# Performance work log

Measured on AMD Instinct MI355X. Metric: run time of the kernel, lower is better.

The kernel has to match this reference:

```python
import jax, jax.numpy as jnp
import numpy as np

N_NODES = 50000
N_EDGES = 800000
IN_DIM = 128
HID = 256
HEADS = 4
OUT_DIM = 128
NEG_SLOPE = 0.2


def gat_conv(x, src, dst, W, a_src, a_dst, b, heads, out_ch):
    """PyG-style GATConv: per-edge attention + segment softmax over dst."""
    N = x.shape[0]
    h = (x @ W).reshape(N, heads, out_ch)              # [N,H,C]
    alph_s = jnp.einsum('nhc,hc->nh', h, a_src)        # [N,H]
    alph_d = jnp.einsum('nhc,hc->nh', h, a_dst)        # [N,H]
    e = jax.nn.leaky_relu(alph_s[src] + alph_d[dst], NEG_SLOPE)  # [E,H]
    m = jax.lax.stop_gradient(jax.ops.segment_max(e, dst, num_segments=N))
    ex = jnp.exp(e - m[dst])
    s = jax.ops.segment_sum(ex, dst, num_segments=N)
    alpha = ex / (s[dst] + 1e-16)                      # [E,H]
    out = jax.ops.segment_sum(h[src] * alpha[:, :, None], dst, num_segments=N)
    return out.reshape(N, heads * out_ch) + b


def setup_inputs() -> dict:
    key = jax.random.key(0)
    ks = jax.random.split(key, 12)
    x = jax.random.normal(ks[0], (N_NODES, IN_DIM), dtype=jnp.float32)
    edge_index = jax.random.randint(ks[1], (2, N_EDGES), 0, N_NODES, dtype=jnp.int64)
    c1 = HID // HEADS  # 64
    sc1 = 1.0 / np.sqrt(IN_DIM)
    sc2 = 1.0 / np.sqrt(HID)
    W1 = jax.random.normal(ks[2], (IN_DIM, HID), dtype=jnp.float32) * sc1
    a1_src = jax.random.normal(ks[3], (HEADS, c1), dtype=jnp.float32) * sc1
    a1_dst = jax.random.normal(ks[4], (HEADS, c1), dtype=jnp.float32) * sc1
    b1 = jnp.zeros((HID,), dtype=jnp.float32)
    W2 = jax.random.normal(ks[5], (HID, OUT_DIM), dtype=jnp.float32) * sc2
    a2_src = jax.random.normal(ks[6], (1, OUT_DIM), dtype=jnp.float32) * sc2
    a2_dst = jax.random.normal(ks[7], (1, OUT_DIM), dtype=jnp.float32) * sc2
    b2 = jnp.zeros((OUT_DIM,), dtype=jnp.float32)
    return {"x": x, "edge_index": edge_index, "W1": W1, "a1_src": a1_src,
            "a1_dst": a1_dst, "b1": b1, "W2": W2, "a2_src": a2_src,
            "a2_dst": a2_dst, "b2": b2}


def reference(x, edge_index, W1, a1_src, a1_dst, b1, W2, a2_src, a2_dst, b2):
    N = x.shape[0]
    loops = jnp.arange(N, dtype=edge_index.dtype)
    # PyG default add_self_loops=True
    src = jnp.concatenate([edge_index[0], loops])
    dst = jnp.concatenate([edge_index[1], loops])
    h = jax.nn.relu(gat_conv(x, src, dst, W1, a1_src, a1_dst, b1, HEADS, HID // HEADS))
    # dropout is identity in eval mode
    return gat_conv(h, src, dst, W2, a2_src, a2_dst, b2, 1, OUT_DIM)
```

## Files before the change

kernel.cpp:

```cpp
#include <hip/hip_runtime.h>
#include <math.h>

#define NEG_SLOPE 0.2f
#define SLOTS 64
#define ECAP 63
#define NBMAX 391
#define BCAP 2432

typedef __attribute__((ext_vector_type(8))) short bf16x8;
typedef __attribute__((ext_vector_type(4))) float f32x4;
typedef __attribute__((ext_vector_type(2))) float f32x2;

__device__ __forceinline__ float lrelu(float t) {
    return t > 0.f ? t : NEG_SLOPE * t;
}
__device__ __forceinline__ unsigned short f2bf(float f) {
    unsigned u = __float_as_uint(f);
    unsigned r = (u + 0x7fff + ((u >> 16) & 1)) >> 16;
    return (unsigned short)r;
}
__device__ __forceinline__ f32x2 unpack2(unsigned v) {
    f32x2 r;
    r.x = __uint_as_float(v << 16);
    r.y = __uint_as_float(v & 0xffff0000u);
    return r;
}

__global__ void prep0(const float* __restrict__ W1, const float* __restrict__ a1s,
                      const float* __restrict__ a1d, float* __restrict__ vsd1,
                      const float* __restrict__ W2, const float* __restrict__ a2s,
                      const float* __restrict__ a2d, float* __restrict__ vsd2) {
    int i = blockIdx.x * 256 + threadIdx.x;
    if (i < 512) {
        int k = i >> 2, h = i & 3;
        float s = 0.f, d = 0.f;
        for (int c = 0; c < 64; c++) {
            float wv = W1[k * 256 + h * 64 + c];
            s += wv * a1s[h * 64 + c];
            d += wv * a1d[h * 64 + c];
        }
        vsd1[h * 128 + k] = s;
        vsd1[(4 + h) * 128 + k] = d;
    } else if (i < 768) {
        int j = i - 512;
        float s = 0.f, d = 0.f;
        for (int c = 0; c < 128; c++) {
            float wv = W2[j * 128 + c];
            s += wv * a2s[c];
            d += wv * a2d[c];
        }
        vsd2[j] = s;
        vsd2[256 + j] = d;
    }
}

#define EMIT(dd, ss)                                                     \
    {                                                                    \
        int bk_ = (dd) >> 7;                                             \
        int pos_ = atomicAdd(&cntS[bk_], 1);                             \
        if (pos_ < BCAP)                                                 \
            bin[(size_t)bk_ * BCAP + pos_] =                             \
                ((unsigned)((dd) & 127) << 16) | (unsigned)(ss);         \
    }

__global__ void mega(const int* __restrict__ src, const int* __restrict__ dst,
                     int* __restrict__ gcur, unsigned* __restrict__ bin,
                     const float* __restrict__ x, uint4* __restrict__ xb4,
                     const float* __restrict__ W1, unsigned short* __restrict__ W1t,
                     const float* __restrict__ W2, unsigned short* __restrict__ W2t,
                     const float* __restrict__ vsd1,
                     float* __restrict__ as1, float* __restrict__ ad1,
                     int E, int N, int nb, int bP1, int bC, int bW1, int bW2) {
    __shared__ float vs[1024];
    __shared__ int cntS[NBMAX];
    const int b = blockIdx.x, t = threadIdx.x;
    if (b < bP1) {
        for (int i = t; i < nb; i += 256) cntS[i] = 0;
        __syncthreads();
        const int4* s4p = (const int4*)src;
        const int4* d4p = (const int4*)dst;
        const int E4 = E >> 2;
        int4 sv[4], dv[4];
        bool act[4];
#pragma unroll
        for (int i = 0; i < 4; i++) {
            int idx = b * 1024 + i * 256 + t;
            act[i] = idx < E4;
            sv[i] = act[i] ? s4p[idx] : (int4){0, 0, 0, 0};
            dv[i] = act[i] ? d4p[idx] : (int4){0, 0, 0, 0};
        }
        int exd = -1, exs = 0;
        if (b == 0 && (E4 << 2) + t < E) {
            exd = dst[(E4 << 2) + t];
            exs = src[(E4 << 2) + t];
        }
#pragma unroll
        for (int i = 0; i < 4; i++)
            if (act[i]) {
                atomicAdd(&cntS[dv[i].x >> 7], 1);
                atomicAdd(&cntS[dv[i].y >> 7], 1);
                atomicAdd(&cntS[dv[i].z >> 7], 1);
                atomicAdd(&cntS[dv[i].w >> 7], 1);
            }
        if (exd >= 0) atomicAdd(&cntS[exd >> 7], 1);
        __syncthreads();
        for (int i = t; i < nb; i += 256) {
            int c = cntS[i];
            cntS[i] = c ? atomicAdd(&gcur[i], c) : 0;
        }
        __syncthreads();
#pragma unroll
        for (int i = 0; i < 4; i++)
            if (act[i]) {
                EMIT(dv[i].x, sv[i].x);
                EMIT(dv[i].y, sv[i].y);
                EMIT(dv[i].z, sv[i].z);
                EMIT(dv[i].w, sv[i].w);
            }
        if (exd >= 0) EMIT(exd, exs);
    } else if (b < bC) {
        int i = (b - bP1) * 256 + t;
        if (i < N * 16) {
            const float4* x4 = (const float4*)x;
            float4 v0 = x4[2 * i], v1 = x4[2 * i + 1];
            uint4 o;
            o.x = (unsigned)f2bf(v0.x) | ((unsigned)f2bf(v0.y) << 16);
            o.y = (unsigned)f2bf(v0.z) | ((unsigned)f2bf(v0.w) << 16);
            o.z = (unsigned)f2bf(v1.x) | ((unsigned)f2bf(v1.y) << 16);
            o.w = (unsigned)f2bf(v1.z) | ((unsigned)f2bf(v1.w) << 16);
            xb4[i] = o;
        }
    } else if (b < bW1) {
        int i = (b - bC) * 256 + t;
        int n = i >> 7, k = i & 127;
        W1t[i] = f2bf(W1[k * 256 + n]);
    } else if (b < bW2) {
        int i = (b - bW1) * 256 + t;
        int n = i >> 8, k = i & 255;
        W2t[i] = f2bf(W2[k * 128 + n]);
    } else {
        for (int i = t; i < 1024; i += 256) vs[i] = vsd1[i];
        __syncthreads();
        int wave = t >> 6, lane = t & 63;
        int n = (b - bW2) * 4 + wave;
        if (n >= N) return;
        float acc[8];
#pragma unroll
        for (int j = 0; j < 8; j++) acc[j] = 0.f;
#pragma unroll
        for (int i = 0; i < 2; i++) {
            float xv = x[(size_t)n * 128 + i * 64 + lane];
#pragma unroll
            for (int j = 0; j < 8; j++) acc[j] += xv * vs[j * 128 + i * 64 + lane];
        }
#pragma unroll
        for (int off = 32; off > 0; off >>= 1) {
#pragma unroll
            for (int j = 0; j < 8; j++) acc[j] += __shfl_down(acc[j], off, 64);
        }
        if (lane == 0) {
#pragma unroll
            for (int h = 0; h < 4; h++) {
                as1[n * 4 + h] = acc[h];
                ad1[n * 4 + h] = acc[4 + h];
            }
        }
    }
}

__global__ __launch_bounds__(256) void build_csr(const int* __restrict__ gcur,
                                                 const unsigned* __restrict__ bin,
                                                 unsigned short* __restrict__ eSrc,
                                                 int* __restrict__ cursor) {
    __shared__ unsigned short slotS[128 * 64];
    __shared__ int lc[128];
    const int b = blockIdx.x, t = threadIdx.x;
    if (t < 128) lc[t] = 0;
    __syncthreads();
    int cnt = gcur[b];
    if (cnt > BCAP) cnt = BCAP;
    const unsigned* bb = bin + (size_t)b * BCAP;
    for (int i = t; i < cnt; i += 256) {
        unsigned e = bb[i];
        int dl = e >> 16;
        int p = atomicAdd(&lc[dl], 1);
        if (p < ECAP) slotS[(dl << 6) + p] = (unsigned short)(e & 0xffff);
    }
    __syncthreads();
    const uint4* sp = (const uint4*)slotS;
    uint4* dp = (uint4*)(eSrc + ((size_t)b << 13));
#pragma unroll
    for (int i = 0; i < 4; i++) dp[t + i * 256] = sp[t + i * 256];
    if (t < 128) cursor[(b << 7) + t] = lc[t];
}

template <int K, int N>
__global__ __launch_bounds__(256) void gemm_mfma(const unsigned short* __restrict__ A,
                                                 const unsigned short* __restrict__ Bt,
                                                 unsigned short* __restrict__ Cb, int M) {
    constexpr int LDT = 72;
    __shared__ __align__(16) short As[128 * LDT];
    __shared__ __align__(16) short Bs[64 * LDT];
    const int t = threadIdx.x;
    const int wave = t >> 6, lane = t & 63;
    const int row0 = blockIdx.x * 128;
    const int n0 = blockIdx.y * 64;

    f32x4 acc[2][4];
#pragma unroll
    for (int mt = 0; mt < 2; mt++)
#pragma unroll
        for (int nt = 0; nt < 4; nt++) acc[mt][nt] = (f32x4){0.f, 0.f, 0.f, 0.f};

    const int r = t >> 3, c8 = (t & 7) * 8;
    for (int kc = 0; kc < K; kc += 64) {
        const unsigned short* srcA = A + (size_t)row0 * K + kc;
#pragma unroll
        for (int p = 0; p < 4; p++) {
            int rr = r + p * 32;
            *(bf16x8*)&As[rr * LDT + c8] = *(const bf16x8*)&srcA[(size_t)rr * K + c8];
        }
        const unsigned short* srcB = Bt + (size_t)n0 * K + kc;
#pragma unroll
        for (int p = 0; p < 2; p++) {
            int rr = r + p * 32;
            *(bf16x8*)&Bs[rr * LDT + c8] = *(const bf16x8*)&srcB[(size_t)rr * K + c8];
        }
        __syncthreads();

        const int mbase = wave * 32 + (lane & 15);
        const int quad = lane >> 4;
#pragma unroll
        for (int ks = 0; ks < 2; ks++) {
            int ko = ks * 32 + quad * 8;
            bf16x8 a0 = *(const bf16x8*)&As[mbase * LDT + ko];
            bf16x8 a1 = *(const bf16x8*)&As[(mbase + 16) * LDT + ko];
#pragma unroll
            for (int nt = 0; nt < 4; nt++) {
                bf16x8 b = *(const bf16x8*)&Bs[((lane & 15) + nt * 16) * LDT + ko];
                acc[0][nt] = __builtin_amdgcn_mfma_f32_16x16x32_bf16(a0, b, acc[0][nt], 0, 0, 0);
                acc[1][nt] = __builtin_amdgcn_mfma_f32_16x16x32_bf16(a1, b, acc[1][nt], 0, 0, 0);
            }
        }
        __syncthreads();
    }

    const int colb = n0 + (lane & 15);
    const int rquad = (lane >> 4) * 4;
#pragma unroll
    for (int mt = 0; mt < 2; mt++) {
        int rb = row0 + wave * 32 + mt * 16 + rquad;
#pragma unroll
        for (int nt = 0; nt < 4; nt++) {
#pragma unroll
            for (int rr2 = 0; rr2 < 4; rr2++) {
                int row = rb + rr2;
                if (row < M) Cb[(size_t)row * N + colb + nt * 16] = f2bf(acc[mt][nt][rr2]);
            }
        }
    }
}

__global__ __launch_bounds__(256) void gemm1_head(
    const unsigned short* __restrict__ agg, const unsigned short* __restrict__ W1t,
    const float* __restrict__ b1, const float* __restrict__ vsd2,
    unsigned short* __restrict__ out1b, float* __restrict__ as2, float* __restrict__ ad2,
    int M, int Mpad) {
    constexpr int K = 128, LDT = 72;
    __shared__ __align__(16) short As[128 * LDT];
    __shared__ __align__(16) short Bs[64 * LDT];
    const int t = threadIdx.x;
    const int wave = t >> 6, lane = t & 63;
    const int row0 = blockIdx.x * 128;
    const int h = blockIdx.y;
    const unsigned short* A = agg + (size_t)h * Mpad * K;
    const unsigned short* Bt = W1t + (size_t)h * 64 * K;

    f32x4 acc[2][4];
#pragma unroll
    for (int mt = 0; mt < 2; mt++)
#pragma unroll
        for (int nt = 0; nt < 4; nt++) acc[mt][nt] = (f32x4){0.f, 0.f, 0.f, 0.f};

    const int r = t >> 3, c8 = (t & 7) * 8;
    for (int kc = 0; kc < K; kc += 64) {
        const unsigned short* srcA = A + (size_t)row0 * K + kc;
#pragma unroll
        for (int p = 0; p < 4; p++) {
            int rr = r + p * 32;
            *(bf16x8*)&As[rr * LDT + c8] = *(const bf16x8*)&srcA[(size_t)rr * K + c8];
        }
        const unsigned short* srcB = Bt + kc;
#pragma unroll
        for (int p = 0; p < 2; p++) {
            int rr = r + p * 32;
            *(bf16x8*)&Bs[rr * LDT + c8] = *(const bf16x8*)&srcB[(size_t)rr * K + c8];
        }
        __syncthreads();

        const int mbase = wave * 32 + (lane & 15);
        const int quad = lane >> 4;
#pragma unroll
        for (int ks = 0; ks < 2; ks++) {
            int ko = ks * 32 + quad * 8;
            bf16x8 a0 = *(const bf16x8*)&As[mbase * LDT + ko];
            bf16x8 a1 = *(const bf16x8*)&As[(mbase + 16) * LDT + ko];
#pragma unroll
            for (int nt = 0; nt < 4; nt++) {
                bf16x8 b = *(const bf16x8*)&Bs[((lane & 15) + nt * 16) * LDT + ko];
                acc[0][nt] = __builtin_amdgcn_mfma_f32_16x16x32_bf16(a0, b, acc[0][nt], 0, 0, 0);
                acc[1][nt] = __builtin_amdgcn_mfma_f32_16x16x32_bf16(a1, b, acc[1][nt], 0, 0, 0);
            }
        }
        __syncthreads();
    }

    const int col16 = lane & 15;
    const int grp = lane >> 4;
#pragma unroll
    for (int mt = 0; mt < 2; mt++) {
        int rb = row0 + wave * 32 + mt * 16 + grp * 4;
#pragma unroll
        for (int rr = 0; rr < 4; rr++) {
            int row = rb + rr;
            float ps = 0.f, pd = 0.f;
#pragma unroll
            for (int nt = 0; nt < 4; nt++) {
                int cg = h * 64 + col16 + nt * 16;
                float rres = acc[mt][nt][rr] + b1[cg];
                rres = fmaxf(rres, 0.f);
                if (row < M) out1b[(size_t)row * 256 + cg] = f2bf(rres);
                ps += rres * vsd2[cg];
                pd += rres * vsd2[256 + cg];
            }
#pragma unroll
            for (int mask = 1; mask < 16; mask <<= 1) {
                ps += __shfl_xor(ps, mask, 64);
                pd += __shfl_xor(pd, mask, 64);
            }
            if (col16 == 0 && row < M) {
                atomicAdd(&as2[row], ps);
                atomicAdd(&ad2[row], pd);
            }
        }
    }
}

__global__ __launch_bounds__(256) void fused_gather1(
    const int* __restrict__ cursor, const unsigned short* __restrict__ eSrc,
    const unsigned short* __restrict__ Xb,
    const float* __restrict__ as_, const float* __restrict__ ad_,
    unsigned short* __restrict__ agg, int N, int Mpad) {
    const int wv = threadIdx.x >> 6, lane = threadIdx.x & 63;
    const int half = lane >> 5, hl = lane & 31;
    const int d = blockIdx.x * 8 + wv * 2 + half;

    __shared__ float4 alS[4][2][64];
    __shared__ int offS[4][2][64];

    const bool vn = d < N;
    int deg = 0;
    if (vn) { deg = cursor[d]; if (deg > ECAP) deg = ECAP; }
    float4 adv = make_float4(0.f, 0.f, 0.f, 0.f);
    if (vn) adv = ((const float4*)ad_)[d];

    const int beg = d << 6;
    const int j0 = hl, j1 = hl + 32;
    const bool a0 = vn && (j0 <= deg), a1 = vn && (j1 <= deg);
    int s0 = vn ? d : 0, s1 = vn ? d : 0;
    if (vn && j0 < deg) s0 = eSrc[beg + j0];
    if (vn && j1 < deg) s1 = eSrc[beg + j1];
    float4 q0 = make_float4(0.f, 0.f, 0.f, 0.f), q1 = q0;
    if (a0) q0 = ((const float4*)as_)[s0];
    if (a1) q1 = ((const float4*)as_)[s1];

    float qa0[4] = {q0.x, q0.y, q0.z, q0.w};
    float qa1[4] = {q1.x, q1.y, q1.z, q1.w};
    float ad4[4] = {adv.x, adv.y, adv.z, adv.w};
    float e0[4], e1[4], m[4];
#pragma unroll
    for (int h = 0; h < 4; h++) {
        e0[h] = a0 ? lrelu(qa0[h] + ad4[h]) : -1e30f;
        e1[h] = a1 ? lrelu(qa1[h] + ad4[h]) : -1e30f;
        m[h] = fmaxf(e0[h], e1[h]);
    }
#pragma unroll
    for (int off = 1; off < 32; off <<= 1)
#pragma unroll
        for (int h = 0; h < 4; h++) m[h] = fmaxf(m[h], __shfl_xor(m[h], off, 64));
    float x0[4], x1[4], sum[4];
#pragma unroll
    for (int h = 0; h < 4; h++) {
        x0[h] = a0 ? __expf(e0[h] - m[h]) : 0.f;
        x1[h] = a1 ? __expf(e1[h] - m[h]) : 0.f;
        sum[h] = x0[h] + x1[h];
    }
#pragma unroll
    for (int off = 1; off < 32; off <<= 1)
#pragma unroll
        for (int h = 0; h < 4; h++) sum[h] += __shfl_xor(sum[h], off, 64);
    float ri[4];
#pragma unroll
    for (int h = 0; h < 4; h++) ri[h] = 1.f / (sum[h] + 1e-16f);

    alS[wv][half][j0] = make_float4(x0[0] * ri[0], x0[1] * ri[1], x0[2] * ri[2], x0[3] * ri[3]);
    alS[wv][half][j1] = make_float4(x1[0] * ri[0], x1[1] * ri[1], x1[2] * ri[2], x1[3] * ri[3]);
    offS[wv][half][j0] = s0 << 8;
    offS[wv][half][j1] = s1 << 8;

    int rows = vn ? deg + 1 : 0;
    { int o = __shfl_xor(rows, 32, 64); rows = rows > o ? rows : o; }

    const char* Xc = (const char*)Xb;
    const int myoff = hl * 8;
    f32x2 acc[4][2];
#pragma unroll
    for (int h = 0; h < 4; h++) { acc[h][0] = (f32x2){0.f, 0.f}; acc[h][1] = (f32x2){0.f, 0.f}; }

    int j = 0;
    for (; j + 3 < rows; j += 4) {
        int o0 = offS[wv][half][j], o1 = offS[wv][half][j + 1];
        int o2 = offS[wv][half][j + 2], o3 = offS[wv][half][j + 3];
        uint2 v0 = *(const uint2*)(Xc + o0 + myoff);
        uint2 v1 = *(const uint2*)(Xc + o1 + myoff);
        uint2 v2 = *(const uint2*)(Xc + o2 + myoff);
        uint2 v3 = *(const uint2*)(Xc + o3 + myoff);
        float4 al0 = alS[wv][half][j];
        float4 al1 = alS[wv][half][j + 1];
        float4 al2 = alS[wv][half][j + 2];
        float4 al3 = alS[wv][half][j + 3];
        {
            f32x2 lo = unpack2(v0.x), hi = unpack2(v0.y);
            acc[0][0] += al0.x * lo; acc[0][1] += al0.x * hi;
            acc[1][0] += al0.y * lo; acc[1][1] += al0.y * hi;
            acc[2][0] += al0.z * lo; acc[2][1] += al0.z * hi;
            acc[3][0] += al0.w * lo; acc[3][1] += al0.w * hi;
        }
        {
            f32x2 lo = unpack2(v1.x), hi = unpack2(v1.y);
            acc[0][0] += al1.x * lo; acc[0][1] += al1.x * hi;
            acc[1][0] += al1.y * lo; acc[1][1] += al1.y * hi;
            acc[2][0] += al1.z * lo; acc[2][1] += al1.z * hi;
            acc[3][0] += al1.w * lo; acc[3][1] += al1.w * hi;
        }
        {
            f32x2 lo = unpack2(v2.x), hi = unpack2(v2.y);
            acc[0][0] += al2.x * lo; acc[0][1] += al2.x * hi;
            acc[1][0] += al2.y * lo; acc[1][1] += al2.y * hi;
            acc[2][0] += al2.z * lo; acc[2][1] += al2.z * hi;
            acc[3][0] += al2.w * lo; acc[3][1] += al2.w * hi;
        }
        {
            f32x2 lo = unpack2(v3.x), hi = unpack2(v3.y);
            acc[0][0] += al3.x * lo; acc[0][1] += al3.x * hi;
            acc[1][0] += al3.y * lo; acc[1][1] += al3.y * hi;
            acc[2][0] += al3.z * lo; acc[2][1] += al3.z * hi;
            acc[3][0] += al3.w * lo; acc[3][1] += al3.w * hi;
        }
    }
    for (; j < rows; j++) {
        int o0 = offS[wv][half][j];
        uint2 v0 = *(const uint2*)(Xc + o0 + myoff);
        float4 al0 = alS[wv][half][j];
        f32x2 lo = unpack2(v0.x), hi = unpack2(v0.y);
        acc[0][0] += al0.x * lo; acc[0][1] += al0.x * hi;
        acc[1][0] += al0.y * lo; acc[1][1] += al0.y * hi;
        acc[2][0] += al0.z * lo; acc[2][1] += al0.z * hi;
        acc[3][0] += al0.w * lo; acc[3][1] += al0.w * hi;
    }

    if (vn) {
#pragma unroll
        for (int h = 0; h < 4; h++) {
            uint2 pack;
            pack.x = (unsigned)f2bf(acc[h][0].x) | ((unsigned)f2bf(acc[h][0].y) << 16);
            pack.y = (unsigned)f2bf(acc[h][1].x) | ((unsigned)f2bf(acc[h][1].y) << 16);
            ((uint2*)(agg + ((size_t)h * Mpad + d) * 128))[hl] = pack;
        }
    }
}

__global__ __launch_bounds__(256) void fused_gather2(
    const int* __restrict__ cursor, const unsigned short* __restrict__ eSrc,
    const unsigned short* __restrict__ Hb,
    const float* __restrict__ as_, const float* __restrict__ ad_,
    const float* __restrict__ b2, float* __restrict__ out, int N) {
    const int wv = threadIdx.x >> 6, lane = threadIdx.x & 63;
    const int half = lane >> 5, hl = lane & 31;
    const int d = blockIdx.x * 8 + wv * 2 + half;

    __shared__ float alS[4][2][64];
    __shared__ int offS[4][2][64];

    const bool vn = d < N;
    int deg = 0;
    if (vn) { deg = cursor[d]; if (deg > ECAP) deg = ECAP; }
    const float adv = vn ? ad_[d] : 0.f;

    const int beg = d << 6;
    const int j0 = hl, j1 = hl + 32;
    const bool a0 = vn && (j0 <= deg), a1 = vn && (j1 <= deg);
    int s0 = vn ? d : 0, s1 = vn ? d : 0;
    if (vn && j0 < deg) s0 = eSrc[beg + j0];
    if (vn && j1 < deg) s1 = eSrc[beg + j1];
    float e0 = a0 ? lrelu(as_[s0] + adv) : -1e30f;
    float e1 = a1 ? lrelu(as_[s1] + adv) : -1e30f;
    float m = fmaxf(e0, e1);
#pragma unroll
    for (int off = 1; off < 32; off <<= 1) m = fmaxf(m, __shfl_xor(m, off, 64));
    float x0 = a0 ? __expf(e0 - m) : 0.f;
    float x1 = a1 ? __expf(e1 - m) : 0.f;
    float sum = x0 + x1;
#pragma unroll
    for (int off = 1; off < 32; off <<= 1) sum += __shfl_xor(sum, off, 64);
    float ri = 1.f / (sum + 1e-16f);

    alS[wv][half][j0] = x0 * ri;
    alS[wv][half][j1] = x1 * ri;
    offS[wv][half][j0] = s0 << 8;
    offS[wv][half][j1] = s1 << 8;

    int rows = vn ? deg + 1 : 0;
    { int o = __shfl_xor(rows, 32, 64); rows = rows > o ? rows : o; }

    const char* Hc = (const char*)Hb;
    const int myoff = hl * 8;
    f32x2 acc0 = (f32x2){0.f, 0.f}, acc1 = (f32x2){0.f, 0.f};

    int j = 0;
    for (; j + 3 < rows; j += 4) {
        int o0 = offS[wv][half][j], o1 = offS[wv][half][j + 1];
        int o2 = offS[wv][half][j + 2], o3 = offS[wv][half][j + 3];
        uint2 v0 = *(const uint2*)(Hc + o0 + myoff);
        uint2 v1 = *(const uint2*)(Hc + o1 + myoff);
        uint2 v2 = *(const uint2*)(Hc + o2 + myoff);
        uint2 v3 = *(const uint2*)(Hc + o3 + myoff);
        float b0 = alS[wv][half][j], b1v = alS[wv][half][j + 1];
        float b2v = alS[wv][half][j + 2], b3 = alS[wv][half][j + 3];
        acc0 += b0 * unpack2(v0.x); acc1 += b0 * unpack2(v0.y);
        acc0 += b1v * unpack2(v1.x); acc1 += b1v * unpack2(v1.y);
        acc0 += b2v * unpack2(v2.x); acc1 += b2v * unpack2(v2.y);
        acc0 += b3 * unpack2(v3.x); acc1 += b3 * unpack2(v3.y);
    }
    for (; j < rows; j++) {
        int o0 = offS[wv][half][j];
        uint2 v0 = *(const uint2*)(Hc + o0 + myoff);
        float b0 = alS[wv][half][j];
        acc0 += b0 * unpack2(v0.x); acc1 += b0 * unpack2(v0.y);
    }

    if (vn) {
        float4 bb = ((const float4*)b2)[hl];
        float4 o;
        o.x = acc0.x + bb.x;
        o.y = acc0.y + bb.y;
        o.z = acc1.x + bb.z;
        o.w = acc1.y + bb.w;
        ((float4*)(out + (size_t)d * 128))[hl] = o;
    }
}

extern "C" void kernel_launch(void* const* d_in, const int* in_sizes, int n_in,
                              void* d_out, int out_size, void* d_ws, size_t ws_size,
                              hipStream_t stream) {
    const float* x   = (const float*)d_in[0];
    const int*   ei  = (const int*)d_in[1];
    const float* W1  = (const float*)d_in[2];
    const float* a1s = (const float*)d_in[3];
    const float* a1d = (const float*)d_in[4];
    const float* b1  = (const float*)d_in[5];
    const float* W2  = (const float*)d_in[6];
    const float* a2s = (const float*)d_in[7];
    const float* a2d = (const float*)d_in[8];
    const float* b2  = (const float*)d_in[9];

    const int N = in_sizes[0] / 128;
    const int E = in_sizes[1] / 2;
    const int* srcIdx = ei;
    const int* dstIdx = ei + E;
    float* out = (float*)d_out;

    const int MT = (N + 127) / 128;
    const int M_pad = MT * 128;
    const int nb = (N + 127) >> 7;

    char* w = (char*)d_ws;
    unsigned short* x_bf  = (unsigned short*)w; w += (size_t)N * 128 * 2;
    unsigned short* agg   = (unsigned short*)w; w += (size_t)4 * M_pad * 128 * 2;
    unsigned short* out1b = (unsigned short*)w; w += (size_t)M_pad * 256 * 2;
    unsigned short* h2b   = (unsigned short*)w; w += (size_t)N * 128 * 2;
    unsigned short* W1t   = (unsigned short*)w; w += (size_t)128 * 256 * 2;
    unsigned short* W2t   = (unsigned short*)w; w += (size_t)256 * 128 * 2;
    float* vsd1 = (float*)w; w += (size_t)128 * 8 * 4;
    float* vsd2 = (float*)w; w += (size_t)256 * 2 * 4;
    float* as1  = (float*)w; w += (size_t)N * 4 * 4;
    float* ad1  = (float*)w; w += (size_t)N * 4 * 4;
    float* as2  = (float*)w; w += (size_t)N * 4;
    float* ad2  = (float*)w; w += (size_t)N * 4;
    int* cursor = (int*)w;  w += (size_t)M_pad * 4;
    unsigned short* eSrc = (unsigned short*)w; w += (size_t)M_pad * SLOTS * 2;
    int* gcur = (int*)w; w += (size_t)nb * 4;
    unsigned* bin = (unsigned*)agg;

    hipMemsetAsync(gcur, 0, (size_t)nb * 4, stream);
    hipMemsetAsync(as2, 0, (size_t)N * 4, stream);
    hipMemsetAsync(ad2, 0, (size_t)N * 4, stream);

    prep0<<<3, 256, 0, stream>>>(W1, a1s, a1d, vsd1, W2, a2s, a2d, vsd2);

    {
        const int bP1 = (E / 4 + 1023) / 1024;
        const int nC  = (N * 16 + 255) / 256;
        const int bC  = bP1 + nC;
        const int bW1 = bC + 128;
        const int bW2 = bW1 + 128;
        const int nG  = (N + 3) / 4;
        mega<<<bW2 + nG, 256, 0, stream>>>(srcIdx, dstIdx, gcur, bin,
                                           x, (uint4*)x_bf, W1, W1t, W2, W2t,
                                           vsd1, as1, ad1, E, N, nb, bP1, bC, bW1, bW2);
    }

    build_csr<<<nb, 256, 0, stream>>>(gcur, bin, eSrc, cursor);

    fused_gather1<<<(N + 7) / 8, 256, 0, stream>>>(cursor, eSrc, x_bf, as1, ad1, agg, N, M_pad);
    gemm1_head<<<dim3(MT, 4), 256, 0, stream>>>(agg, W1t, b1, vsd2, out1b, as2, ad2, N, M_pad);

    gemm_mfma<256, 128><<<dim3(MT, 2), 256, 0, stream>>>(out1b, W2t, h2b, N);
    fused_gather2<<<(N + 7) / 8, 256, 0, stream>>>(cursor, eSrc, h2b, as2, ad2, b2, out, N);
}
```

Before: 249.1 us.

## Fuse layer-1 gather with its head GEMM and shrink edge-binning blocks

Merges the layer-1 attention gather and the per-head W1 GEMM into one kernel. Each block gathers 32 destination rows for all four heads into shared memory, then runs MFMA against W1t read directly from global memory, with the bias, ReLU and layer-2 attention projections in the epilogue. This removes the round trip through the 4×Mpad×128 bf16 agg buffer and one kernel launch, so the edge bin now aliases out1b. The edge-binning part of the mega kernel also moves from four int4 per thread to one, which quadruples the block count and the number of global atomics on gcur in exchange for more parallelism.

```diff
diff --git a/kernel.cpp b/kernel.cpp
--- a/kernel.cpp
+++ b/kernel.cpp
@@ -80,28 +80,21 @@
         const int4* s4p = (const int4*)src;
         const int4* d4p = (const int4*)dst;
         const int E4 = E >> 2;
-        int4 sv[4], dv[4];
-        bool act[4];
-#pragma unroll
-        for (int i = 0; i < 4; i++) {
-            int idx = b * 1024 + i * 256 + t;
-            act[i] = idx < E4;
-            sv[i] = act[i] ? s4p[idx] : (int4){0, 0, 0, 0};
-            dv[i] = act[i] ? d4p[idx] : (int4){0, 0, 0, 0};
-        }
+        const int idx = b * 256 + t;
+        const bool act = idx < E4;
+        int4 sv = act ? s4p[idx] : (int4){0, 0, 0, 0};
+        int4 dv = act ? d4p[idx] : (int4){0, 0, 0, 0};
         int exd = -1, exs = 0;
         if (b == 0 && (E4 << 2) + t < E) {
             exd = dst[(E4 << 2) + t];
             exs = src[(E4 << 2) + t];
         }
-#pragma unroll
-        for (int i = 0; i < 4; i++)
-            if (act[i]) {
-                atomicAdd(&cntS[dv[i].x >> 7], 1);
-                atomicAdd(&cntS[dv[i].y >> 7], 1);
-                atomicAdd(&cntS[dv[i].z >> 7], 1);
-                atomicAdd(&cntS[dv[i].w >> 7], 1);
-            }
+        if (act) {
+            atomicAdd(&cntS[dv.x >> 7], 1);
+            atomicAdd(&cntS[dv.y >> 7], 1);
+            atomicAdd(&cntS[dv.z >> 7], 1);
+            atomicAdd(&cntS[dv.w >> 7], 1);
+        }
         if (exd >= 0) atomicAdd(&cntS[exd >> 7], 1);
         __syncthreads();
         for (int i = t; i < nb; i += 256) {
@@ -109,14 +102,12 @@
             cntS[i] = c ? atomicAdd(&gcur[i], c) : 0;
         }
         __syncthreads();
-#pragma unroll
-        for (int i = 0; i < 4; i++)
-            if (act[i]) {
-                EMIT(dv[i].x, sv[i].x);
-                EMIT(dv[i].y, sv[i].y);
-                EMIT(dv[i].z, sv[i].z);
-                EMIT(dv[i].w, sv[i].w);
-            }
+        if (act) {
+            EMIT(dv.x, sv.x);
+            EMIT(dv.y, sv.y);
+            EMIT(dv.z, sv.z);
+            EMIT(dv.w, sv.w);
+        }
         if (exd >= 0) EMIT(exd, exs);
     } else if (b < bC) {
         int i = (b - bP1) * 256 + t;
@@ -194,6 +185,202 @@
     if (t < 128) cursor[(b << 7) + t] = lc[t];
 }
 
+__global__ __launch_bounds__(256) void gather_gemm1(
+    const int* __restrict__ cursor, const unsigned short* __restrict__ eSrc,
+    const unsigned short* __restrict__ Xb,
+    const float* __restrict__ as_, const float* __restrict__ ad_,
+    const unsigned short* __restrict__ W1t, const float* __restrict__ b1,
+    const float* __restrict__ vsd2,
+    unsigned short* __restrict__ out1b, float* __restrict__ as2,
+    float* __restrict__ ad2, int N) {
+    constexpr int LDT = 136;
+    __shared__ __align__(16) short As[128 * LDT];
+    __shared__ float4 alS[4][2][64];
+    __shared__ int offS[4][2][64];
+    const int t = threadIdx.x;
+    const int wv = t >> 6, lane = t & 63;
+    const int half = lane >> 5, hl = lane & 31;
+    const int row0 = blockIdx.x * 32;
+
+    for (int pass = 0; pass < 4; pass++) {
+        const int ln = pass * 8 + wv * 2 + half;
+        const int d = row0 + ln;
+        const bool vn = d < N;
+        int deg = 0;
+        if (vn) { deg = cursor[d]; if (deg > ECAP) deg = ECAP; }
+        float4 adv = make_float4(0.f, 0.f, 0.f, 0.f);
+        if (vn) adv = ((const float4*)ad_)[d];
+
+        const int beg = d << 6;
+        const int j0 = hl, j1 = hl + 32;
+        const bool a0 = vn && (j0 <= deg), a1 = vn && (j1 <= deg);
+        int s0 = vn ? d : 0, s1 = vn ? d : 0;
+        if (vn && j0 < deg) s0 = eSrc[beg + j0];
+        if (vn && j1 < deg) s1 = eSrc[beg + j1];
+        float4 q0 = make_float4(0.f, 0.f, 0.f, 0.f), q1 = q0;
+        if (a0) q0 = ((const float4*)as_)[s0];
+        if (a1) q1 = ((const float4*)as_)[s1];
+
+        float qa0[4] = {q0.x, q0.y, q0.z, q0.w};
+        float qa1[4] = {q1.x, q1.y, q1.z, q1.w};
+        float ad4[4] = {adv.x, adv.y, adv.z, adv.w};
+        float e0[4], e1[4], m[4];
+#pragma unroll
+        for (int h = 0; h < 4; h++) {
+            e0[h] = a0 ? lrelu(qa0[h] + ad4[h]) : -1e30f;
+            e1[h] = a1 ? lrelu(qa1[h] + ad4[h]) : -1e30f;
+            m[h] = fmaxf(e0[h], e1[h]);
+        }
+#pragma unroll
+        for (int off = 1; off < 32; off <<= 1)
+#pragma unroll
+            for (int h = 0; h < 4; h++) m[h] = fmaxf(m[h], __shfl_xor(m[h], off, 64));
+        float x0[4], x1[4], sum[4];
+#pragma unroll
+        for (int h = 0; h < 4; h++) {
+            x0[h] = a0 ? __expf(e0[h] - m[h]) : 0.f;
+            x1[h] = a1 ? __expf(e1[h] - m[h]) : 0.f;
+            sum[h] = x0[h] + x1[h];
+        }
+#pragma unroll
+        for (int off = 1; off < 32; off <<= 1)
+#pragma unroll
+            for (int h = 0; h < 4; h++) sum[h] += __shfl_xor(sum[h], off, 64);
+        float ri[4];
+#pragma unroll
+        for (int h = 0; h < 4; h++) ri[h] = 1.f / (sum[h] + 1e-16f);
+
+        alS[wv][half][j0] = make_float4(x0[0] * ri[0], x0[1] * ri[1], x0[2] * ri[2], x0[3] * ri[3]);
+        alS[wv][half][j1] = make_float4(x1[0] * ri[0], x1[1] * ri[1], x1[2] * ri[2], x1[3] * ri[3]);
+        offS[wv][half][j0] = s0 << 8;
+        offS[wv][half][j1] = s1 << 8;
+
+        int rows = vn ? deg + 1 : 0;
+        { int o = __shfl_xor(rows, 32, 64); rows = rows > o ? rows : o; }
+
+        const char* Xc = (const char*)Xb;
+        const int myoff = hl * 8;
+        f32x2 acc[4][2];
+#pragma unroll
+        for (int h = 0; h < 4; h++) { acc[h][0] = (f32x2){0.f, 0.f}; acc[h][1] = (f32x2){0.f, 0.f}; }
+
+        int j = 0;
+        for (; j + 3 < rows; j += 4) {
+            int o0 = offS[wv][half][j], o1 = offS[wv][half][j + 1];
+            int o2 = offS[wv][half][j + 2], o3 = offS[wv][half][j + 3];
+            uint2 v0 = *(const uint2*)(Xc + o0 + myoff);
+            uint2 v1 = *(const uint2*)(Xc + o1 + myoff);
+            uint2 v2 = *(const uint2*)(Xc + o2 + myoff);
+            uint2 v3 = *(const uint2*)(Xc + o3 + myoff);
+            float4 al0 = alS[wv][half][j];
+            float4 al1 = alS[wv][half][j + 1];
+            float4 al2 = alS[wv][half][j + 2];
+            float4 al3 = alS[wv][half][j + 3];
+            {
+                f32x2 lo = unpack2(v0.x), hi = unpack2(v0.y);
+                acc[0][0] += al0.x * lo; acc[0][1] += al0.x * hi;
+                acc[1][0] += al0.y * lo; acc[1][1] += al0.y * hi;
+                acc[2][0] += al0.z * lo; acc[2][1] += al0.z * hi;
+                acc[3][0] += al0.w * lo; acc[3][1] += al0.w * hi;
+            }
+            {
+                f32x2 lo = unpack2(v1.x), hi = unpack2(v1.y);
+                acc[0][0] += al1.x * lo; acc[0][1] += al1.x * hi;
+                acc[1][0] += al1.y * lo; acc[1][1] += al1.y * hi;
+                acc[2][0] += al1.z * lo; acc[2][1] += al1.z * hi;
+                acc[3][0] += al1.w * lo; acc[3][1] += al1.w * hi;
+            }
+            {
+                f32x2 lo = unpack2(v2.x), hi = unpack2(v2.y);
+                acc[0][0] += al2.x * lo; acc[0][1] += al2.x * hi;
+                acc[1][0] += al2.y * lo; acc[1][1] += al2.y * hi;
+                acc[2][0] += al2.z * lo; acc[2][1] += al2.z * hi;
+                acc[3][0] += al2.w * lo; acc[3][1] += al2.w * hi;
+            }
+            {
+                f32x2 lo = unpack2(v3.x), hi = unpack2(v3.y);
+                acc[0][0] += al3.x * lo; acc[0][1] += al3.x * hi;
+                acc[1][0] += al3.y * lo; acc[1][1] += al3.y * hi;
+                acc[2][0] += al3.z * lo; acc[2][1] += al3.z * hi;
+                acc[3][0] += al3.w * lo; acc[3][1] += al3.w * hi;
+            }
+        }
+        for (; j < rows; j++) {
+            int o0 = offS[wv][half][j];
+            uint2 v0 = *(const uint2*)(Xc + o0 + myoff);
+            float4 al0 = alS[wv][half][j];
+            f32x2 lo = unpack2(v0.x), hi = unpack2(v0.y);
+            acc[0][0] += al0.x * lo; acc[0][1] += al0.x * hi;
+            acc[1][0] += al0.y * lo; acc[1][1] += al0.y * hi;
+            acc[2][0] += al0.z * lo; acc[2][1] += al0.z * hi;
+            acc[3][0] += al0.w * lo; acc[3][1] += al0.w * hi;
+        }
+
+        if (vn) {
+#pragma unroll
+            for (int h = 0; h < 4; h++) {
+                uint2 pack;
+                pack.x = (unsigned)f2bf(acc[h][0].x) | ((unsigned)f2bf(acc[h][0].y) << 16);
+                pack.y = (unsigned)f2bf(acc[h][1].x) | ((unsigned)f2bf(acc[h][1].y) << 16);
+                ((uint2*)&As[(h * 32 + ln) * LDT])[hl] = pack;
+            }
+        }
+    }
+    __syncthreads();
+
+    const int h = wv;
+    const short* Ah = &As[h * 32 * LDT];
+    const unsigned short* Bh = W1t + (size_t)h * 64 * 128;
+    const int l16 = lane & 15, quad = lane >> 4;
+
+    f32x4 acc[2][4];
+#pragma unroll
+    for (int mt = 0; mt < 2; mt++)
+#pragma unroll
+        for (int nt = 0; nt < 4; nt++) acc[mt][nt] = (f32x4){0.f, 0.f, 0.f, 0.f};
+
+#pragma unroll
+    for (int ks = 0; ks < 4; ks++) {
+        const int ko = ks * 32 + quad * 8;
+        bf16x8 a0 = *(const bf16x8*)&Ah[l16 * LDT + ko];
+        bf16x8 a1 = *(const bf16x8*)&Ah[(16 + l16) * LDT + ko];
+#pragma unroll
+        for (int nt = 0; nt < 4; nt++) {
+            bf16x8 b = *(const bf16x8*)&Bh[(size_t)(nt * 16 + l16) * 128 + ko];
+            acc[0][nt] = __builtin_amdgcn_mfma_f32_16x16x32_bf16(a0, b, acc[0][nt], 0, 0, 0);
+            acc[1][nt] = __builtin_amdgcn_mfma_f32_16x16x32_bf16(a1, b, acc[1][nt], 0, 0, 0);
+        }
+    }
+
+#pragma unroll
+    for (int mt = 0; mt < 2; mt++) {
+        int rb = row0 + mt * 16 + quad * 4;
+#pragma unroll
+        for (int rr = 0; rr < 4; rr++) {
+            int row = rb + rr;
+            float ps = 0.f, pd = 0.f;
+#pragma unroll
+            for (int nt = 0; nt < 4; nt++) {
+                int cg = h * 64 + l16 + nt * 16;
+                float rres = acc[mt][nt][rr] + b1[cg];
+                rres = fmaxf(rres, 0.f);
+                if (row < N) out1b[(size_t)row * 256 + cg] = f2bf(rres);
+                ps += rres * vsd2[cg];
+                pd += rres * vsd2[256 + cg];
+            }
+#pragma unroll
+            for (int mask = 1; mask < 16; mask <<= 1) {
+                ps += __shfl_xor(ps, mask, 64);
+                pd += __shfl_xor(pd, mask, 64);
+            }
+            if (l16 == 0 && row < N) {
+                atomicAdd(&as2[row], ps);
+                atomicAdd(&ad2[row], pd);
+            }
+        }
+    }
+}
+
 template <int K, int N>
 __global__ __launch_bounds__(256) void gemm_mfma(const unsigned short* __restrict__ A,
                                                  const unsigned short* __restrict__ Bt,
@@ -257,225 +444,6 @@
                 int row = rb + rr2;
                 if (row < M) Cb[(size_t)row * N + colb + nt * 16] = f2bf(acc[mt][nt][rr2]);
             }
-        }
-    }
-}
-
-__global__ __launch_bounds__(256) void gemm1_head(
-    const unsigned short* __restrict__ agg, const unsigned short* __restrict__ W1t,
-    const float* __restrict__ b1, const float* __restrict__ vsd2,
-    unsigned short* __restrict__ out1b, float* __restrict__ as2, float* __restrict__ ad2,
-    int M, int Mpad) {
-    constexpr int K = 128, LDT = 72;
-    __shared__ __align__(16) short As[128 * LDT];
-    __shared__ __align__(16) short Bs[64 * LDT];
-    const int t = threadIdx.x;
-    const int wave = t >> 6, lane = t & 63;
-    const int row0 = blockIdx.x * 128;
-    const int h = blockIdx.y;
-    const unsigned short* A = agg + (size_t)h * Mpad * K;
-    const unsigned short* Bt = W1t + (size_t)h * 64 * K;
-
-    f32x4 acc[2][4];
-#pragma unroll
-    for (int mt = 0; mt < 2; mt++)
-#pragma unroll
-        for (int nt = 0; nt < 4; nt++) acc[mt][nt] = (f32x4){0.f, 0.f, 0.f, 0.f};
-
-    const int r = t >> 3, c8 = (t & 7) * 8;
-    for (int kc = 0; kc < K; kc += 64) {
-        const unsigned short* srcA = A + (size_t)row0 * K + kc;
-#pragma unroll
-        for (int p = 0; p < 4; p++) {
-            int rr = r + p * 32;
-            *(bf16x8*)&As[rr * LDT + c8] = *(const bf16x8*)&srcA[(size_t)rr * K + c8];
-        }
-        const unsigned short* srcB = Bt + kc;
-#pragma unroll
-        for (int p = 0; p < 2; p++) {
-            int rr = r + p * 32;
-            *(bf16x8*)&Bs[rr * LDT + c8] = *(const bf16x8*)&srcB[(size_t)rr * K + c8];
-        }
-        __syncthreads();
-
-        const int mbase = wave * 32 + (lane & 15);
-        const int quad = lane >> 4;
-#pragma unroll
-        for (int ks = 0; ks < 2; ks++) {
-            int ko = ks * 32 + quad * 8;
-            bf16x8 a0 = *(const bf16x8*)&As[mbase * LDT + ko];
-            bf16x8 a1 = *(const bf16x8*)&As[(mbase + 16) * LDT + ko];
-#pragma unroll
-            for (int nt = 0; nt < 4; nt++) {
-                bf16x8 b = *(const bf16x8*)&Bs[((lane & 15) + nt * 16) * LDT + ko];
-                acc[0][nt] = __builtin_amdgcn_mfma_f32_16x16x32_bf16(a0, b, acc[0][nt], 0, 0, 0);
-                acc[1][nt] = __builtin_amdgcn_mfma_f32_16x16x32_bf16(a1, b, acc[1][nt], 0, 0, 0);
-            }
-        }
-        __syncthreads();
-    }
-
-    const int col16 = lane & 15;
-    const int grp = lane >> 4;
-#pragma unroll
-    for (int mt = 0; mt < 2; mt++) {
-        int rb = row0 + wave * 32 + mt * 16 + grp * 4;
-#pragma unroll
-        for (int rr = 0; rr < 4; rr++) {
-            int row = rb + rr;
-            float ps = 0.f, pd = 0.f;
-#pragma unroll
-            for (int nt = 0; nt < 4; nt++) {
-                int cg = h * 64 + col16 + nt * 16;
-                float rres = acc[mt][nt][rr] + b1[cg];
-                rres = fmaxf(rres, 0.f);
-                if (row < M) out1b[(size_t)row * 256 + cg] = f2bf(rres);
-                ps += rres * vsd2[cg];
-                pd += rres * vsd2[256 + cg];
-            }
-#pragma unroll
-            for (int mask = 1; mask < 16; mask <<= 1) {
-                ps += __shfl_xor(ps, mask, 64);
-                pd += __shfl_xor(pd, mask, 64);
-            }
-            if (col16 == 0 && row < M) {
-                atomicAdd(&as2[row], ps);
-                atomicAdd(&ad2[row], pd);
-            }
-        }
-    }
-}
-
-__global__ __launch_bounds__(256) void fused_gather1(
-    const int* __restrict__ cursor, const unsigned short* __restrict__ eSrc,
-    const unsigned short* __restrict__ Xb,
-    const float* __restrict__ as_, const float* __restrict__ ad_,
-    unsigned short* __restrict__ agg, int N, int Mpad) {
-    const int wv = threadIdx.x >> 6, lane = threadIdx.x & 63;
-    const int half = lane >> 5, hl = lane & 31;
-    const int d = blockIdx.x * 8 + wv * 2 + half;
-
-    __shared__ float4 alS[4][2][64];
-    __shared__ int offS[4][2][64];
-
-    const bool vn = d < N;
-    int deg = 0;
-    if (vn) { deg = cursor[d]; if (deg > ECAP) deg = ECAP; }
-    float4 adv = make_float4(0.f, 0.f, 0.f, 0.f);
-    if (vn) adv = ((const float4*)ad_)[d];
-
-    const int beg = d << 6;
-    const int j0 = hl, j1 = hl + 32;
-    const bool a0 = vn && (j0 <= deg), a1 = vn && (j1 <= deg);
-    int s0 = vn ? d : 0, s1 = vn ? d : 0;
-    if (vn && j0 < deg) s0 = eSrc[beg + j0];
-    if (vn && j1 < deg) s1 = eSrc[beg + j1];
-    float4 q0 = make_float4(0.f, 0.f, 0.f, 0.f), q1 = q0;
-    if (a0) q0 = ((const float4*)as_)[s0];
-    if (a1) q1 = ((const float4*)as_)[s1];
-
-    float qa0[4] = {q0.x, q0.y, q0.z, q0.w};
-    float qa1[4] = {q1.x, q1.y, q1.z, q1.w};
-    float ad4[4] = {adv.x, adv.y, adv.z, adv.w};
-    float e0[4], e1[4], m[4];
-#pragma unroll
-    for (int h = 0; h < 4; h++) {
-        e0[h] = a0 ? lrelu(qa0[h] + ad4[h]) : -1e30f;
-        e1[h] = a1 ? lrelu(qa1[h] + ad4[h]) : -1e30f;
-        m[h] = fmaxf(e0[h], e1[h]);
-    }
-#pragma unroll
-    for (int off = 1; off < 32; off <<= 1)
-#pragma unroll
-        for (int h = 0; h < 4; h++) m[h] = fmaxf(m[h], __shfl_xor(m[h], off, 64));
-    float x0[4], x1[4], sum[4];
-#pragma unroll
-    for (int h = 0; h < 4; h++) {
-        x0[h] = a0 ? __expf(e0[h] - m[h]) : 0.f;
-        x1[h] = a1 ? __expf(e1[h] - m[h]) : 0.f;
-        sum[h] = x0[h] + x1[h];
-    }
-#pragma unroll
-    for (int off = 1; off < 32; off <<= 1)
-#pragma unroll
-        for (int h = 0; h < 4; h++) sum[h] += __shfl_xor(sum[h], off, 64);
-    float ri[4];
-#pragma unroll
-    for (int h = 0; h < 4; h++) ri[h] = 1.f / (sum[h] + 1e-16f);
-
-    alS[wv][half][j0] = make_float4(x0[0] * ri[0], x0[1] * ri[1], x0[2] * ri[2], x0[3] * ri[3]);
-    alS[wv][half][j1] = make_float4(x1[0] * ri[0], x1[1] * ri[1], x1[2] * ri[2], x1[3] * ri[3]);
-    offS[wv][half][j0] = s0 << 8;
-    offS[wv][half][j1] = s1 << 8;
-
-    int rows = vn ? deg + 1 : 0;
-    { int o = __shfl_xor(rows, 32, 64); rows = rows > o ? rows : o; }
-
-    const char* Xc = (const char*)Xb;
-    const int myoff = hl * 8;
-    f32x2 acc[4][2];
-#pragma unroll
-    for (int h = 0; h < 4; h++) { acc[h][0] = (f32x2){0.f, 0.f}; acc[h][1] = (f32x2){0.f, 0.f}; }
-
-    int j = 0;
-    for (; j + 3 < rows; j += 4) {
-        int o0 = offS[wv][half][j], o1 = offS[wv][half][j + 1];
-        int o2 = offS[wv][half][j + 2], o3 = offS[wv][half][j + 3];
-        uint2 v0 = *(const uint2*)(Xc + o0 + myoff);
-        uint2 v1 = *(const uint2*)(Xc + o1 + myoff);
-        uint2 v2 = *(const uint2*)(Xc + o2 + myoff);
-        uint2 v3 = *(const uint2*)(Xc + o3 + myoff);
-        float4 al0 = alS[wv][half][j];
-        float4 al1 = alS[wv][half][j + 1];
-        float4 al2 = alS[wv][half][j + 2];
-        float4 al3 = alS[wv][half][j + 3];
-        {
-            f32x2 lo = unpack2(v0.x), hi = unpack2(v0.y);
-            acc[0][0] += al0.x * lo; acc[0][1] += al0.x * hi;
-            acc[1][0] += al0.y * lo; acc[1][1] += al0.y * hi;
-            acc[2][0] += al0.z * lo; acc[2][1] += al0.z * hi;
-            acc[3][0] += al0.w * lo; acc[3][1] += al0.w * hi;
-        }
-        {
-            f32x2 lo = unpack2(v1.x), hi = unpack2(v1.y);
-            acc[0][0] += al1.x * lo; acc[0][1] += al1.x * hi;
-            acc[1][0] += al1.y * lo; acc[1][1] += al1.y * hi;
-            acc[2][0] += al1.z * lo; acc[2][1] += al1.z * hi;
-            acc[3][0] += al1.w * lo; acc[3][1] += al1.w * hi;
-        }
-        {
-            f32x2 lo = unpack2(v2.x), hi = unpack2(v2.y);
-            acc[0][0] += al2.x * lo; acc[0][1] += al2.x * hi;
-            acc[1][0] += al2.y * lo; acc[1][1] += al2.y * hi;
-            acc[2][0] += al2.z * lo; acc[2][1] += al2.z * hi;
-            acc[3][0] += al2.w * lo; acc[3][1] += al2.w * hi;
-        }
-        {
-            f32x2 lo = unpack2(v3.x), hi = unpack2(v3.y);
-            acc[0][0] += al3.x * lo; acc[0][1] += al3.x * hi;
-            acc[1][0] += al3.y * lo; acc[1][1] += al3.y * hi;
-            acc[2][0] += al3.z * lo; acc[2][1] += al3.z * hi;
-            acc[3][0] += al3.w * lo; acc[3][1] += al3.w * hi;
-        }
-    }
-    for (; j < rows; j++) {
-        int o0 = offS[wv][half][j];
-        uint2 v0 = *(const uint2*)(Xc + o0 + myoff);
-        float4 al0 = alS[wv][half][j];
-        f32x2 lo = unpack2(v0.x), hi = unpack2(v0.y);
-        acc[0][0] += al0.x * lo; acc[0][1] += al0.x * hi;
-        acc[1][0] += al0.y * lo; acc[1][1] += al0.y * hi;
-        acc[2][0] += al0.z * lo; acc[2][1] += al0.z * hi;
-        acc[3][0] += al0.w * lo; acc[3][1] += al0.w * hi;
-    }
-
-    if (vn) {
-#pragma unroll
-        for (int h = 0; h < 4; h++) {
-            uint2 pack;
-            pack.x = (unsigned)f2bf(acc[h][0].x) | ((unsigned)f2bf(acc[h][0].y) << 16);
-            pack.y = (unsigned)f2bf(acc[h][1].x) | ((unsigned)f2bf(acc[h][1].y) << 16);
-            ((uint2*)(agg + ((size_t)h * Mpad + d) * 128))[hl] = pack;
         }
     }
 }
@@ -586,7 +554,6 @@
 
     char* w = (char*)d_ws;
     unsigned short* x_bf  = (unsigned short*)w; w += (size_t)N * 128 * 2;
-    unsigned short* agg   = (unsigned short*)w; w += (size_t)4 * M_pad * 128 * 2;
     unsigned short* out1b = (unsigned short*)w; w += (size_t)M_pad * 256 * 2;
     unsigned short* h2b   = (unsigned short*)w; w += (size_t)N * 128 * 2;
     unsigned short* W1t   = (unsigned short*)w; w += (size_t)128 * 256 * 2;
@@ -600,7 +567,7 @@
     int* cursor = (int*)w;  w += (size_t)M_pad * 4;
     unsigned short* eSrc = (unsigned short*)w; w += (size_t)M_pad * SLOTS * 2;
     int* gcur = (int*)w; w += (size_t)nb * 4;
-    unsigned* bin = (unsigned*)agg;
+    unsigned* bin = (unsigned*)out1b;
 
     hipMemsetAsync(gcur, 0, (size_t)nb * 4, stream);
     hipMemsetAsync(as2, 0, (size_t)N * 4, stream);
@@ -609,7 +576,7 @@
     prep0<<<3, 256, 0, stream>>>(W1, a1s, a1d, vsd1, W2, a2s, a2d, vsd2);
 
     {
-        const int bP1 = (E / 4 + 1023) / 1024;
+        const int bP1 = (E / 4 + 255) / 256;
         const int nC  = (N * 16 + 255) / 256;
         const int bC  = bP1 + nC;
         const int bW1 = bC + 128;
@@ -622,8 +589,8 @@
 
     build_csr<<<nb, 256, 0, stream>>>(gcur, bin, eSrc, cursor);
 
-    fused_gather1<<<(N + 7) / 8, 256, 0, stream>>>(cursor, eSrc, x_bf, as1, ad1, agg, N, M_pad);
-    gemm1_head<<<dim3(MT, 4), 256, 0, stream>>>(agg, W1t, b1, vsd2, out1b, as2, ad2, N, M_pad);
+    gather_gemm1<<<(N + 31) / 32, 256, 0, stream>>>(cursor, eSrc, x_bf, as1, ad1,
+                                                    W1t, b1, vsd2, out1b, as2, ad2, N);
 
     gemm_mfma<256, 128><<<dim3(MT, 2), 256, 0, stream>>>(out1b, W2t, h2b, N);
     fused_gather2<<<(N + 7) / 8, 256, 0, stream>>>(cursor, eSrc, h2b, as2, ad2, b2, out, N);
```

Result: slower. 294.8 us (+18.3%).

## Fold memsets into prep kernel and regroup binning, CSR build and conversions

Applied to the files above, without the earlier changes.

Replaces three hipMemsetAsync calls with zeroing blocks inside the prep kernel. Binning moves out of the mixed kernel into its own kernel with one int4 per thread instead of four, which launches more blocks. The CSR build is merged with the x/W conversion and attention-logit work into one launch. Together these cut the launch count and let the independent conversion work overlap with the CSR build, at the cost of more global atomics on gcur from the smaller binning blocks and larger shared-memory use in the merged kernel.

```diff
diff --git a/kernel.cpp b/kernel.cpp
--- a/kernel.cpp
+++ b/kernel.cpp
@@ -26,31 +26,41 @@
     return r;
 }
 
-__global__ void prep0(const float* __restrict__ W1, const float* __restrict__ a1s,
-                      const float* __restrict__ a1d, float* __restrict__ vsd1,
-                      const float* __restrict__ W2, const float* __restrict__ a2s,
-                      const float* __restrict__ a2d, float* __restrict__ vsd2) {
-    int i = blockIdx.x * 256 + threadIdx.x;
-    if (i < 512) {
-        int k = i >> 2, h = i & 3;
-        float s = 0.f, d = 0.f;
-        for (int c = 0; c < 64; c++) {
-            float wv = W1[k * 256 + h * 64 + c];
-            s += wv * a1s[h * 64 + c];
-            d += wv * a1d[h * 64 + c];
-        }
-        vsd1[h * 128 + k] = s;
-        vsd1[(4 + h) * 128 + k] = d;
-    } else if (i < 768) {
-        int j = i - 512;
-        float s = 0.f, d = 0.f;
-        for (int c = 0; c < 128; c++) {
-            float wv = W2[j * 128 + c];
-            s += wv * a2s[c];
-            d += wv * a2d[c];
-        }
-        vsd2[j] = s;
-        vsd2[256 + j] = d;
+__global__ void prep(const float* __restrict__ W1, const float* __restrict__ a1s,
+                     const float* __restrict__ a1d, float* __restrict__ vsd1,
+                     const float* __restrict__ W2, const float* __restrict__ a2s,
+                     const float* __restrict__ a2d, float* __restrict__ vsd2,
+                     float* __restrict__ as2, float* __restrict__ ad2,
+                     int* __restrict__ gcur, int N, int nb) {
+    const int b = blockIdx.x, t = threadIdx.x;
+    if (b < 3) {
+        int i = b * 256 + t;
+        if (i < 512) {
+            int k = i >> 2, h = i & 3;
+            float s = 0.f, d = 0.f;
+            for (int c = 0; c < 64; c++) {
+                float wv = W1[k * 256 + h * 64 + c];
+                s += wv * a1s[h * 64 + c];
+                d += wv * a1d[h * 64 + c];
+            }
+            vsd1[h * 128 + k] = s;
+            vsd1[(4 + h) * 128 + k] = d;
+        } else if (i < 768) {
+            int j = i - 512;
+            float s = 0.f, d = 0.f;
+            for (int c = 0; c < 128; c++) {
+                float wv = W2[j * 128 + c];
+                s += wv * a2s[c];
+                d += wv * a2d[c];
+            }
+            vsd2[j] = s;
+            vsd2[256 + j] = d;
+        }
+    } else {
+        int i = (b - 3) * 256 + t;
+        if (i < N) as2[i] = 0.f;
+        else if (i < 2 * N) ad2[i - N] = 0.f;
+        else if (i < 2 * N + nb) gcur[i - 2 * N] = 0;
     }
 }
 
@@ -63,63 +73,80 @@
                 ((unsigned)((dd) & 127) << 16) | (unsigned)(ss);         \
     }
 
-__global__ void mega(const int* __restrict__ src, const int* __restrict__ dst,
-                     int* __restrict__ gcur, unsigned* __restrict__ bin,
+__global__ __launch_bounds__(256) void bink(const int* __restrict__ src,
+                                            const int* __restrict__ dst,
+                                            int* __restrict__ gcur,
+                                            unsigned* __restrict__ bin, int E, int nb) {
+    __shared__ int cntS[NBMAX];
+    const int b = blockIdx.x, t = threadIdx.x;
+    for (int i = t; i < nb; i += 256) cntS[i] = 0;
+    __syncthreads();
+    const int4* s4p = (const int4*)src;
+    const int4* d4p = (const int4*)dst;
+    const int E4 = E >> 2;
+    const int idx = b * 256 + t;
+    const bool act = idx < E4;
+    int4 sv = act ? s4p[idx] : (int4){0, 0, 0, 0};
+    int4 dv = act ? d4p[idx] : (int4){0, 0, 0, 0};
+    int exd = -1, exs = 0;
+    if (b == 0 && (E4 << 2) + t < E) {
+        exd = dst[(E4 << 2) + t];
+        exs = src[(E4 << 2) + t];
+    }
+    if (act) {
+        atomicAdd(&cntS[dv.x >> 7], 1);
+        atomicAdd(&cntS[dv.y >> 7], 1);
+        atomicAdd(&cntS[dv.z >> 7], 1);
+        atomicAdd(&cntS[dv.w >> 7], 1);
+    }
+    if (exd >= 0) atomicAdd(&cntS[exd >> 7], 1);
+    __syncthreads();
+    for (int i = t; i < nb; i += 256) {
+        int c = cntS[i];
+        cntS[i] = c ? atomicAdd(&gcur[i], c) : 0;
+    }
+    __syncthreads();
+    if (act) {
+        EMIT(dv.x, sv.x);
+        EMIT(dv.y, sv.y);
+        EMIT(dv.z, sv.z);
+        EMIT(dv.w, sv.w);
+    }
+    if (exd >= 0) EMIT(exd, exs);
+}
+
+__global__ void wmix(const int* __restrict__ gcur, const unsigned* __restrict__ bin,
+                     unsigned short* __restrict__ eSrc, int* __restrict__ cursor,
                      const float* __restrict__ x, uint4* __restrict__ xb4,
                      const float* __restrict__ W1, unsigned short* __restrict__ W1t,
                      const float* __restrict__ W2, unsigned short* __restrict__ W2t,
                      const float* __restrict__ vsd1,
                      float* __restrict__ as1, float* __restrict__ ad1,
-                     int E, int N, int nb, int bP1, int bC, int bW1, int bW2) {
+                     int N, int nb, int bC, int bW1, int bW2) {
+    __shared__ unsigned short slotS[128 * 64];
+    __shared__ int lc[128];
     __shared__ float vs[1024];
-    __shared__ int cntS[NBMAX];
     const int b = blockIdx.x, t = threadIdx.x;
-    if (b < bP1) {
-        for (int i = t; i < nb; i += 256) cntS[i] = 0;
+    if (b < nb) {
+        if (t < 128) lc[t] = 0;
         __syncthreads();
-        const int4* s4p = (const int4*)src;
-        const int4* d4p = (const int4*)dst;
-        const int E4 = E >> 2;
-        int4 sv[4], dv[4];
-        bool act[4];
-#pragma unroll
-        for (int i = 0; i < 4; i++) {
-            int idx = b * 1024 + i * 256 + t;
-            act[i] = idx < E4;
-            sv[i] = act[i] ? s4p[idx] : (int4){0, 0, 0, 0};
-            dv[i] = act[i] ? d4p[idx] : (int4){0, 0, 0, 0};
-        }
-        int exd = -1, exs = 0;
-        if (b == 0 && (E4 << 2) + t < E) {
-            exd = dst[(E4 << 2) + t];
-            exs = src[(E4 << 2) + t];
-        }
-#pragma unroll
-        for (int i = 0; i < 4; i++)
-            if (act[i]) {
-                atomicAdd(&cntS[dv[i].x >> 7], 1);
-                atomicAdd(&cntS[dv[i].y >> 7], 1);
-                atomicAdd(&cntS[dv[i].z >> 7], 1);
-                atomicAdd(&cntS[dv[i].w >> 7], 1);
-            }
-        if (exd >= 0) atomicAdd(&cntS[exd >> 7], 1);
+        int cnt = gcur[b];
+        if (cnt > BCAP) cnt = BCAP;
+        const unsigned* bb = bin + (size_t)b * BCAP;
+        for (int i = t; i < cnt; i += 256) {
+            unsigned e = bb[i];
+            int dl = e >> 16;
+            int p = atomicAdd(&lc[dl], 1);
+            if (p < ECAP) slotS[(dl << 6) + p] = (unsigned short)(e & 0xffff);
+        }
         __syncthreads();
-        for (int i = t; i < nb; i += 256) {
-            int c = cntS[i];
-            cntS[i] = c ? atomicAdd(&gcur[i], c) : 0;
-        }
-        __syncthreads();
-#pragma unroll
-        for (int i = 0; i < 4; i++)
-            if (act[i]) {
-                EMIT(dv[i].x, sv[i].x);
-                EMIT(dv[i].y, sv[i].y);
-                EMIT(dv[i].z, sv[i].z);
-                EMIT(dv[i].w, sv[i].w);
-            }
-        if (exd >= 0) EMIT(exd, exs);
+        const uint4* sp = (const uint4*)slotS;
+        uint4* dp = (uint4*)(eSrc + ((size_t)b << 13));
+#pragma unroll
+        for (int i = 0; i < 4; i++) dp[t + i * 256] = sp[t + i * 256];
+        if (t < 128) cursor[(b << 7) + t] = lc[t];
     } else if (b < bC) {
-        int i = (b - bP1) * 256 + t;
+        int i = (b - nb) * 256 + t;
         if (i < N * 16) {
             const float4* x4 = (const float4*)x;
             float4 v0 = x4[2 * i], v1 = x4[2 * i + 1];
@@ -166,32 +193,6 @@
             }
         }
     }
-}
-
-__global__ __launch_bounds__(256) void build_csr(const int* __restrict__ gcur,
-                                                 const unsigned* __restrict__ bin,
-                                                 unsigned short* __restrict__ eSrc,
-                                                 int* __restrict__ cursor) {
-    __shared__ unsigned short slotS[128 * 64];
-    __shared__ int lc[128];
-    const int b = blockIdx.x, t = threadIdx.x;
-    if (t < 128) lc[t] = 0;
-    __syncthreads();
-    int cnt = gcur[b];
-    if (cnt > BCAP) cnt = BCAP;
-    const unsigned* bb = bin + (size_t)b * BCAP;
-    for (int i = t; i < cnt; i += 256) {
-        unsigned e = bb[i];
-        int dl = e >> 16;
-        int p = atomicAdd(&lc[dl], 1);
-        if (p < ECAP) slotS[(dl << 6) + p] = (unsigned short)(e & 0xffff);
-    }
-    __syncthreads();
-    const uint4* sp = (const uint4*)slotS;
-    uint4* dp = (uint4*)(eSrc + ((size_t)b << 13));
-#pragma unroll
-    for (int i = 0; i < 4; i++) dp[t + i * 256] = sp[t + i * 256];
-    if (t < 128) cursor[(b << 7) + t] = lc[t];
 }
 
 template <int K, int N>
@@ -602,25 +603,24 @@
     int* gcur = (int*)w; w += (size_t)nb * 4;
     unsigned* bin = (unsigned*)agg;
 
-    hipMemsetAsync(gcur, 0, (size_t)nb * 4, stream);
-    hipMemsetAsync(as2, 0, (size_t)N * 4, stream);
-    hipMemsetAsync(ad2, 0, (size_t)N * 4, stream);
-
-    prep0<<<3, 256, 0, stream>>>(W1, a1s, a1d, vsd1, W2, a2s, a2d, vsd2);
-
     {
-        const int bP1 = (E / 4 + 1023) / 1024;
+        const int zb = (2 * N + nb + 255) / 256;
+        prep<<<3 + zb, 256, 0, stream>>>(W1, a1s, a1d, vsd1, W2, a2s, a2d, vsd2,
+                                         as2, ad2, gcur, N, nb);
+    }
+
+    bink<<<(E / 4 + 255) / 256, 256, 0, stream>>>(srcIdx, dstIdx, gcur, bin, E, nb);
+
+    {
         const int nC  = (N * 16 + 255) / 256;
-        const int bC  = bP1 + nC;
+        const int bC  = nb + nC;
         const int bW1 = bC + 128;
         const int bW2 = bW1 + 128;
         const int nG  = (N + 3) / 4;
-        mega<<<bW2 + nG, 256, 0, stream>>>(srcIdx, dstIdx, gcur, bin,
+        wmix<<<bW2 + nG, 256, 0, stream>>>(gcur, bin, eSrc, cursor,
                                            x, (uint4*)x_bf, W1, W1t, W2, W2t,
-                                           vsd1, as1, ad1, E, N, nb, bP1, bC, bW1, bW2);
-    }
-
-    build_csr<<<nb, 256, 0, stream>>>(gcur, bin, eSrc, cursor);
+                                           vsd1, as1, ad1, N, nb, bC, bW1, bW2);
+    }
 
     fused_gather1<<<(N + 7) / 8, 256, 0, stream>>>(cursor, eSrc, x_bf, as1, ad1, agg, N, M_pad);
     gemm1_head<<<dim3(MT, 4), 256, 0, stream>>>(agg, W1t, b1, vsd2, out1b, as2, ad2, N, M_pad);
```

Result: slower. 258.8 us (+3.9%).
